# Optimization experiments

Measured on AMD Instinct MI355X. Metric: run time of the kernel, lower is better.

The kernel has to match this reference:

```python
import jax, jax.numpy as jnp
import numpy as np

N, I, H = 16, 128, 128
B, T = 16, 512


def setup_inputs() -> dict:
    key = jax.random.key(0)
    ks = jax.random.split(key, 6)
    stdv = 1.0 / np.sqrt(H)
    return {
        "x": jax.random.normal(ks[0], (B, T, N * I), dtype=jnp.float32),
        "h_0": jax.random.normal(ks[1], (1, B, N * H), dtype=jnp.float32),
        "weight_ih": jax.random.uniform(ks[2], (N, 3 * H, I), jnp.float32, -stdv, stdv),
        "weight_hh": jax.random.uniform(ks[3], (N, 3 * H, H), jnp.float32, -stdv, stdv),
        "bias_ih": jax.random.uniform(ks[4], (N, 3 * H), jnp.float32, -stdv, stdv),
        "bias_hh": jax.random.uniform(ks[5], (N, 3 * H), jnp.float32, -stdv, stdv),
    }


def reference(x, h_0, weight_ih, weight_hh, bias_ih, bias_hh):
    # x: [B, T, N*I] (batch_first)
    b, t, _ = x.shape
    xr = x.reshape(b, t, N, I)
    # Pre-compute all input projections: [B, T, N, 3H]
    gates_x = jnp.einsum('btni,ngi->btng', xr, weight_ih) + bias_ih[None, None]
    h0 = h_0[0].reshape(b, N, H)  # [B, N, H]

    def step(h, gx):
        # h: [B, N, H]; gx: [B, N, 3H]
        gates_h = jnp.einsum('bnh,ngh->bng', h, weight_hh) + bias_hh[None]
        gx_r, gx_z, gx_n = jnp.split(gx, 3, axis=-1)
        gh_r, gh_z, gh_n = jnp.split(gates_h, 3, axis=-1)
        r = jax.nn.sigmoid(gx_r + gh_r)
        z = jax.nn.sigmoid(gx_z + gh_z)
        n = jnp.tanh(gx_n + r * gh_n)
        h_new = (1 - z) * n + z * h
        return h_new, h_new

    # scan over time: gates_x -> [T, B, N, 3H]
    h_last, hs = jax.lax.scan(step, h0, jnp.swapaxes(gates_x, 0, 1))
    output = jnp.swapaxes(hs, 0, 1).reshape(b, t, N * H)  # [B, T, N*H]
    h_n = h_last.reshape(1, b, N * H)
    return output, h_n
```

## Files before the change

### kernel.cpp

```cpp
#include <hip/hip_runtime.h>
#include <cstdint>
#include <cmath>

#define N_HEADS 16
#define I_DIM 128
#define H_DIM 128
#define B_SZ 16
#define T_SZ 512
#define G3 384
#define BT (B_SZ * T_SZ)
#define LDW 136
#define OUT_HN_OFFSET ((size_t)B_SZ * T_SZ * (N_HEADS * H_DIM))
#define CHUNK 8
#define NCHUNK (T_SZ / CHUNK)

typedef __attribute__((ext_vector_type(8))) short bf16x8;
typedef __attribute__((ext_vector_type(4))) float f32x4;

static __device__ __forceinline__ unsigned short f2bf(float f) {
  unsigned int u = __float_as_uint(f);
  unsigned int r = (u + 0x7FFFu + ((u >> 16) & 1u)) >> 16;
  return (unsigned short)r;
}
static __device__ __forceinline__ float bf2f(unsigned short s) {
  return __uint_as_float((unsigned int)s << 16);
}
static __device__ __forceinline__ uint2 pack4(float4 v) {
  uint2 p;
  p.x = (unsigned int)f2bf(v.x) | ((unsigned int)f2bf(v.y) << 16);
  p.y = (unsigned int)f2bf(v.z) | ((unsigned int)f2bf(v.w) << 16);
  return p;
}
static __device__ __forceinline__ bf16x8 pack8(float4 a, float4 b) {
  union { uint2 u[2]; bf16x8 v; } r;
  r.u[0] = pack4(a);
  r.u[1] = pack4(b);
  return r.v;
}

__global__ __launch_bounds__(256) void gates_x_mfma(
    const float* __restrict__ x, const float* __restrict__ w_ih,
    const float* __restrict__ b_ih, unsigned short* __restrict__ gates) {
  const int n = blockIdx.z;
  const int grp = blockIdx.x;
  const int tid = threadIdx.x;
  const int wave = tid >> 6;
  const int lane = tid & 63;
  const int m16 = lane & 15;
  const int quad = lane >> 4;

  extern __shared__ __align__(16) unsigned short lds_pool[];
  unsigned short* Ws = lds_pool;
  unsigned short* Xs = lds_pool + G3 * LDW;

  const int xrow = tid >> 2;
  const int xq = tid & 3;

  float4 xf[8];
  {
    const float4* xg =
        (const float4*)(x + (size_t)(grp * 512 + xrow) * 2048 + n * I_DIM) +
        xq * 8;
#pragma unroll
    for (int i = 0; i < 8; ++i) xf[i] = xg[i];
  }

  {
    const float4* wsrc = (const float4*)(w_ih + (size_t)n * G3 * I_DIM);
#pragma unroll
    for (int i = 0; i < 48; ++i) {
      const int idx = i * 256 + tid;
      *(uint2*)&Ws[(idx >> 5) * LDW + (idx & 31) * 4] = pack4(wsrc[idx]);
    }
  }

  float bias[3][8];
#pragma unroll
  for (int gb = 0; gb < 3; ++gb)
#pragma unroll
    for (int j = 0; j < 8; ++j)
      bias[gb][j] = b_ih[n * G3 + gb * 128 + j * 16 + m16];

  for (int tile = 0; tile < 8; ++tile) {
    const int bt0 = grp * 512 + tile * 64;

    __syncthreads();
#pragma unroll
    for (int i = 0; i < 8; ++i)
      *(uint2*)&Xs[xrow * LDW + xq * 32 + i * 4] = pack4(xf[i]);
    __syncthreads();

    if (tile < 7) {
      const float4* xg =
          (const float4*)(x + (size_t)(bt0 + 64 + xrow) * 2048 + n * I_DIM) +
          xq * 8;
#pragma unroll
      for (int i = 0; i < 8; ++i) xf[i] = xg[i];
    }

#pragma unroll
    for (int gb = 0; gb < 3; ++gb) {
      f32x4 acc[8];
#pragma unroll
      for (int j = 0; j < 8; ++j) acc[j] = (f32x4){0.f, 0.f, 0.f, 0.f};

#pragma unroll
      for (int kt = 0; kt < 4; ++kt) {
        const bf16x8 afrag =
            *(const bf16x8*)&Xs[(wave * 16 + m16) * LDW + kt * 32 + quad * 8];
#pragma unroll
        for (int j = 0; j < 8; ++j) {
          const bf16x8 bfrag =
              *(const bf16x8*)&Ws[(gb * 128 + j * 16 + m16) * LDW + kt * 32 +
                                  quad * 8];
          acc[j] = __builtin_amdgcn_mfma_f32_16x16x32_bf16(afrag, bfrag,
                                                           acc[j], 0, 0, 0);
        }
      }

#pragma unroll
      for (int j = 0; j < 8; ++j) {
        const int g = gb * 128 + j * 16 + m16;
        float4 v;
        v.x = acc[j][0] + bias[gb][j];
        v.y = acc[j][1] + bias[gb][j];
        v.z = acc[j][2] + bias[gb][j];
        v.w = acc[j][3] + bias[gb][j];
        const int bt = bt0 + wave * 16 + quad * 4;
        *(uint2*)&gates[((size_t)n * G3 + g) * BT + bt] = pack4(v);
      }
    }
  }
}

__global__ __launch_bounds__(256, 1) void gru_scan_kernel(
    const float* __restrict__ h0, const float* __restrict__ w_hh,
    const float* __restrict__ b_hh, const unsigned short* __restrict__ gates,
    float* __restrict__ out) {
  const int b = blockIdx.x >> 4;
  const int n = blockIdx.x & 15;
  const int tid = threadIdx.x;
  const int wave = tid >> 6;
  const int lane = tid & 63;
  const int m16 = lane & 15;
  const int quad = lane >> 4;

  __shared__ __align__(16) unsigned short h2[2][2][H_DIM];
  __shared__ __align__(16) unsigned short gbuf[2][CHUNK * 512];

  bf16x8 wf[6][4];
  {
    const int cb0 = 2 * wave;
    const int cbs[6] = {cb0, 8 + cb0, 16 + cb0, cb0 + 1, 9 + cb0, 17 + cb0};
#pragma unroll
    for (int j = 0; j < 6; ++j) {
      const int g = cbs[j] * 16 + m16;
      const float4* wr = (const float4*)(w_hh + ((size_t)n * G3 + g) * H_DIM);
#pragma unroll
      for (int kt = 0; kt < 4; ++kt)
        wf[j][kt] = pack8(wr[kt * 8 + quad * 2], wr[kt * 8 + quad * 2 + 1]);
    }
  }

  const bool upd = quad < 2;
  const int elem = wave * 32 + quad * 16 + m16;

  float bh_r = 0.f, bh_z = 0.f, bh_n = 0.f, h_old = 0.f;
  if (upd) {
    bh_r = b_hh[n * G3 + elem];
    bh_z = b_hh[n * G3 + elem + 128];
    bh_n = b_hh[n * G3 + elem + 256];
    h_old = h0[(size_t)b * 2048 + n * H_DIM + elem];
    const unsigned short hh = f2bf(h_old);
    h2[0][0][elem] = hh;
    h2[0][1][elem] = f2bf(h_old - bf2f(hh));
  }

  const size_t grow0 = ((size_t)n * G3 + tid) * BT + (size_t)b * T_SZ;
  const size_t grow1 = ((size_t)n * G3 + 256 + tid) * BT + (size_t)b * T_SZ;

  auto scatter = [&](unsigned short* buf, int g, uint4 v) {
    unsigned short* d = buf + (g & 127) * 4 + (g >> 7);
    d[0]    = (unsigned short)v.x;
    d[512]  = (unsigned short)(v.x >> 16);
    d[1024] = (unsigned short)v.y;
    d[1536] = (unsigned short)(v.y >> 16);
    d[2048] = (unsigned short)v.z;
    d[2560] = (unsigned short)(v.z >> 16);
    d[3072] = (unsigned short)v.w;
    d[3584] = (unsigned short)(v.w >> 16);
  };

  uint4 pfA, pfB;
  pfA = *(const uint4*)(gates + grow0);
  if (tid < 128) pfB = *(const uint4*)(gates + grow1);
  scatter(gbuf[0], tid, pfA);
  if (tid < 128) scatter(gbuf[0], 256 + tid, pfB);
  __syncthreads();

  float* out_base = out + (size_t)b * T_SZ * 2048 + n * H_DIM;
  float oreg[CHUNK];

  for (int c = 0; c < NCHUNK; ++c) {
    const int gb = c & 1;

    if (c + 1 < NCHUNK) {
      pfA = *(const uint4*)(gates + grow0 + (size_t)(c + 1) * CHUNK);
      if (tid < 128)
        pfB = *(const uint4*)(gates + grow1 + (size_t)(c + 1) * CHUNK);
    }

#pragma unroll
    for (int s = 0; s < CHUNK; ++s) {
      const int rb = s & 1;
      const int wb = rb ^ 1;

      uint2 gxu = {0u, 0u};
      if (upd) gxu = *(const uint2*)&gbuf[gb][s * 512 + elem * 4];
      const float gxr = __uint_as_float(gxu.x << 16);
      const float gxz = __uint_as_float(gxu.x & 0xffff0000u);
      const float gxn = __uint_as_float(gxu.y << 16);

      const unsigned short* hsrc = &h2[rb][m16 & 1][0];
      const bf16x8 av0 = *(const bf16x8*)&hsrc[0 * 32 + quad * 8];
      const bf16x8 av1 = *(const bf16x8*)&hsrc[1 * 32 + quad * 8];
      const bf16x8 av2 = *(const bf16x8*)&hsrc[2 * 32 + quad * 8];
      const bf16x8 av3 = *(const bf16x8*)&hsrc[3 * 32 + quad * 8];

      f32x4 acc[6];
#pragma unroll
      for (int j = 0; j < 6; ++j) acc[j] = (f32x4){0.f, 0.f, 0.f, 0.f};
#pragma unroll
      for (int j = 0; j < 6; ++j)
        acc[j] = __builtin_amdgcn_mfma_f32_16x16x32_bf16(av0, wf[j][0],
                                                         acc[j], 0, 0, 0);
#pragma unroll
      for (int j = 0; j < 6; ++j)
        acc[j] = __builtin_amdgcn_mfma_f32_16x16x32_bf16(av1, wf[j][1],
                                                         acc[j], 0, 0, 0);
#pragma unroll
      for (int j = 0; j < 6; ++j)
        acc[j] = __builtin_amdgcn_mfma_f32_16x16x32_bf16(av2, wf[j][2],
                                                         acc[j], 0, 0, 0);
#pragma unroll
      for (int j = 0; j < 6; ++j)
        acc[j] = __builtin_amdgcn_mfma_f32_16x16x32_bf16(av3, wf[j][3],
                                                         acc[j], 0, 0, 0);

      if (upd) {
        const float ghr =
            (quad ? acc[3][0] + acc[3][1] : acc[0][0] + acc[0][1]) + bh_r;
        const float ghz =
            (quad ? acc[4][0] + acc[4][1] : acc[1][0] + acc[1][1]) + bh_z;
        const float ghn =
            (quad ? acc[5][0] + acc[5][1] : acc[2][0] + acc[2][1]) + bh_n;
        const float r = 1.f / (1.f + __expf(-(gxr + ghr)));
        const float z = 1.f / (1.f + __expf(-(gxz + ghz)));
        const float targ = gxn + r * ghn;
        const float rt = 1.f / (1.f + __expf(-2.f * targ));
        const float nn = 2.f * rt - 1.f;
        const float hn = (1.f - z) * nn + z * h_old;
        const unsigned short hh = f2bf(hn);
        h2[wb][0][elem] = hh;
        h2[wb][1][elem] = f2bf(hn - bf2f(hh));
        h_old = hn;
        oreg[s] = hn;
      }

      if (s == CHUNK - 1 && c + 1 < NCHUNK) {
        scatter(gbuf[gb ^ 1], tid, pfA);
        if (tid < 128) scatter(gbuf[gb ^ 1], 256 + tid, pfB);
      }
      __syncthreads();
    }

    if (upd) {
#pragma unroll
      for (int s = 0; s < CHUNK; ++s)
        out_base[(size_t)(c * CHUNK + s) * 2048 + elem] = oreg[s];
    }
  }

  if (upd) {
    out[OUT_HN_OFFSET + (size_t)b * 2048 + n * H_DIM + elem] = h_old;
  }
}

extern "C" void kernel_launch(void* const* d_in, const int* in_sizes, int n_in,
                              void* d_out, int out_size, void* d_ws,
                              size_t ws_size, hipStream_t stream) {
  const float* x    = (const float*)d_in[0];
  const float* h0   = (const float*)d_in[1];
  const float* w_ih = (const float*)d_in[2];
  const float* w_hh = (const float*)d_in[3];
  const float* b_ih = (const float*)d_in[4];
  const float* b_hh = (const float*)d_in[5];
  float* out = (float*)d_out;
  unsigned short* gates = (unsigned short*)d_ws;

  static bool lds_opt_in = false;
  if (!lds_opt_in) {
    (void)hipFuncSetAttribute(reinterpret_cast<const void*>(&gates_x_mfma),
                              hipFuncAttributeMaxDynamicSharedMemorySize,
                              (G3 + 64) * LDW * (int)sizeof(unsigned short));
    lds_opt_in = true;
  }

  dim3 gridA(16, 1, N_HEADS);
  gates_x_mfma<<<gridA, 256, (G3 + 64) * LDW * sizeof(unsigned short),
                 stream>>>(x, w_ih, b_ih, gates);
  gru_scan_kernel<<<256, 256, 0, stream>>>(h0, w_hh, b_hh, gates, out);
}
```

Before: 422.7 us.

## Keep input weights in registers and double waves in the scan kernel

```diff
diff --git a/kernel.cpp b/kernel.cpp
--- a/kernel.cpp
+++ b/kernel.cpp
@@ -38,7 +38,7 @@
   return r.v;
 }
 
-__global__ __launch_bounds__(256) void gates_x_mfma(
+__global__ __launch_bounds__(256, 2) void gates_x_mfma(
     const float* __restrict__ x, const float* __restrict__ w_ih,
     const float* __restrict__ b_ih, unsigned short* __restrict__ gates) {
   const int n = blockIdx.z;
@@ -49,9 +49,7 @@
   const int m16 = lane & 15;
   const int quad = lane >> 4;
 
-  extern __shared__ __align__(16) unsigned short lds_pool[];
-  unsigned short* Ws = lds_pool;
-  unsigned short* Xs = lds_pool + G3 * LDW;
+  __shared__ __align__(16) unsigned short Xs[64 * LDW];
 
   const int xrow = tid >> 2;
   const int xq = tid & 3;
@@ -59,30 +57,29 @@
   float4 xf[8];
   {
     const float4* xg =
-        (const float4*)(x + (size_t)(grp * 512 + xrow) * 2048 + n * I_DIM) +
+        (const float4*)(x + (size_t)(grp * 256 + xrow) * 2048 + n * I_DIM) +
         xq * 8;
 #pragma unroll
     for (int i = 0; i < 8; ++i) xf[i] = xg[i];
   }
 
-  {
-    const float4* wsrc = (const float4*)(w_ih + (size_t)n * G3 * I_DIM);
-#pragma unroll
-    for (int i = 0; i < 48; ++i) {
-      const int idx = i * 256 + tid;
-      *(uint2*)&Ws[(idx >> 5) * LDW + (idx & 31) * 4] = pack4(wsrc[idx]);
-    }
-  }
-
-  float bias[3][8];
-#pragma unroll
-  for (int gb = 0; gb < 3; ++gb)
-#pragma unroll
-    for (int j = 0; j < 8; ++j)
-      bias[gb][j] = b_ih[n * G3 + gb * 128 + j * 16 + m16];
-
-  for (int tile = 0; tile < 8; ++tile) {
-    const int bt0 = grp * 512 + tile * 64;
+  bf16x8 wfr[3][2][4];
+  float bias[3][2];
+#pragma unroll
+  for (int gb = 0; gb < 3; ++gb) {
+#pragma unroll
+    for (int jj = 0; jj < 2; ++jj) {
+      const int g = gb * 128 + (2 * wave + jj) * 16 + m16;
+      const float4* wr = (const float4*)(w_ih + ((size_t)n * G3 + g) * I_DIM);
+#pragma unroll
+      for (int kt = 0; kt < 4; ++kt)
+        wfr[gb][jj][kt] = pack8(wr[kt * 8 + quad * 2], wr[kt * 8 + quad * 2 + 1]);
+      bias[gb][jj] = b_ih[n * G3 + g];
+    }
+  }
+
+  for (int tile = 0; tile < 4; ++tile) {
+    const int bt0 = grp * 256 + tile * 64;
 
     __syncthreads();
 #pragma unroll
@@ -90,7 +87,7 @@
       *(uint2*)&Xs[xrow * LDW + xq * 32 + i * 4] = pack4(xf[i]);
     __syncthreads();
 
-    if (tile < 7) {
+    if (tile < 3) {
       const float4* xg =
           (const float4*)(x + (size_t)(bt0 + 64 + xrow) * 2048 + n * I_DIM) +
           xq * 8;
@@ -100,40 +97,45 @@
 
 #pragma unroll
     for (int gb = 0; gb < 3; ++gb) {
-      f32x4 acc[8];
-#pragma unroll
-      for (int j = 0; j < 8; ++j) acc[j] = (f32x4){0.f, 0.f, 0.f, 0.f};
+      f32x4 acc[4][2];
+#pragma unroll
+      for (int m = 0; m < 4; ++m)
+#pragma unroll
+        for (int jj = 0; jj < 2; ++jj) acc[m][jj] = (f32x4){0.f, 0.f, 0.f, 0.f};
 
 #pragma unroll
       for (int kt = 0; kt < 4; ++kt) {
-        const bf16x8 afrag =
-            *(const bf16x8*)&Xs[(wave * 16 + m16) * LDW + kt * 32 + quad * 8];
-#pragma unroll
-        for (int j = 0; j < 8; ++j) {
-          const bf16x8 bfrag =
-              *(const bf16x8*)&Ws[(gb * 128 + j * 16 + m16) * LDW + kt * 32 +
-                                  quad * 8];
-          acc[j] = __builtin_amdgcn_mfma_f32_16x16x32_bf16(afrag, bfrag,
-                                                           acc[j], 0, 0, 0);
+        bf16x8 af[4];
+#pragma unroll
+        for (int m = 0; m < 4; ++m)
+          af[m] = *(const bf16x8*)&Xs[(m * 16 + m16) * LDW + kt * 32 + quad * 8];
+#pragma unroll
+        for (int m = 0; m < 4; ++m)
+#pragma unroll
+          for (int jj = 0; jj < 2; ++jj)
+            acc[m][jj] = __builtin_amdgcn_mfma_f32_16x16x32_bf16(
+                af[m], wfr[gb][jj][kt], acc[m][jj], 0, 0, 0);
+      }
+
+#pragma unroll
+      for (int m = 0; m < 4; ++m) {
+#pragma unroll
+        for (int jj = 0; jj < 2; ++jj) {
+          const int g = gb * 128 + (2 * wave + jj) * 16 + m16;
+          float4 v;
+          v.x = acc[m][jj][0] + bias[gb][jj];
+          v.y = acc[m][jj][1] + bias[gb][jj];
+          v.z = acc[m][jj][2] + bias[gb][jj];
+          v.w = acc[m][jj][3] + bias[gb][jj];
+          const int bt = bt0 + m * 16 + quad * 4;
+          *(uint2*)&gates[((size_t)n * G3 + g) * BT + bt] = pack4(v);
         }
       }
-
-#pragma unroll
-      for (int j = 0; j < 8; ++j) {
-        const int g = gb * 128 + j * 16 + m16;
-        float4 v;
-        v.x = acc[j][0] + bias[gb][j];
-        v.y = acc[j][1] + bias[gb][j];
-        v.z = acc[j][2] + bias[gb][j];
-        v.w = acc[j][3] + bias[gb][j];
-        const int bt = bt0 + wave * 16 + quad * 4;
-        *(uint2*)&gates[((size_t)n * G3 + g) * BT + bt] = pack4(v);
-      }
-    }
-  }
-}
-
-__global__ __launch_bounds__(256, 1) void gru_scan_kernel(
+    }
+  }
+}
+
+__global__ __launch_bounds__(512, 1) void gru_scan_kernel(
     const float* __restrict__ h0, const float* __restrict__ w_hh,
     const float* __restrict__ b_hh, const unsigned short* __restrict__ gates,
     float* __restrict__ out) {
@@ -148,12 +150,11 @@
   __shared__ __align__(16) unsigned short h2[2][2][H_DIM];
   __shared__ __align__(16) unsigned short gbuf[2][CHUNK * 512];
 
-  bf16x8 wf[6][4];
+  bf16x8 wf[3][4];
   {
-    const int cb0 = 2 * wave;
-    const int cbs[6] = {cb0, 8 + cb0, 16 + cb0, cb0 + 1, 9 + cb0, 17 + cb0};
-#pragma unroll
-    for (int j = 0; j < 6; ++j) {
+    const int cbs[3] = {wave, 8 + wave, 16 + wave};
+#pragma unroll
+    for (int j = 0; j < 3; ++j) {
       const int g = cbs[j] * 16 + m16;
       const float4* wr = (const float4*)(w_hh + ((size_t)n * G3 + g) * H_DIM);
 #pragma unroll
@@ -162,8 +163,8 @@
     }
   }
 
-  const bool upd = quad < 2;
-  const int elem = wave * 32 + quad * 16 + m16;
+  const bool upd = (quad == 0);
+  const int elem = wave * 16 + m16;
 
   float bh_r = 0.f, bh_z = 0.f, bh_n = 0.f, h_old = 0.f;
   if (upd) {
@@ -176,8 +177,7 @@
     h2[0][1][elem] = f2bf(h_old - bf2f(hh));
   }
 
-  const size_t grow0 = ((size_t)n * G3 + tid) * BT + (size_t)b * T_SZ;
-  const size_t grow1 = ((size_t)n * G3 + 256 + tid) * BT + (size_t)b * T_SZ;
+  const size_t grow = ((size_t)n * G3 + tid) * BT + (size_t)b * T_SZ;
 
   auto scatter = [&](unsigned short* buf, int g, uint4 v) {
     unsigned short* d = buf + (g & 127) * 4 + (g >> 7);
@@ -191,11 +191,11 @@
     d[3584] = (unsigned short)(v.w >> 16);
   };
 
-  uint4 pfA, pfB;
-  pfA = *(const uint4*)(gates + grow0);
-  if (tid < 128) pfB = *(const uint4*)(gates + grow1);
-  scatter(gbuf[0], tid, pfA);
-  if (tid < 128) scatter(gbuf[0], 256 + tid, pfB);
+  uint4 pfA = {0, 0, 0, 0};
+  if (tid < G3) {
+    pfA = *(const uint4*)(gates + grow);
+    scatter(gbuf[0], tid, pfA);
+  }
   __syncthreads();
 
   float* out_base = out + (size_t)b * T_SZ * 2048 + n * H_DIM;
@@ -204,11 +204,8 @@
   for (int c = 0; c < NCHUNK; ++c) {
     const int gb = c & 1;
 
-    if (c + 1 < NCHUNK) {
-      pfA = *(const uint4*)(gates + grow0 + (size_t)(c + 1) * CHUNK);
-      if (tid < 128)
-        pfB = *(const uint4*)(gates + grow1 + (size_t)(c + 1) * CHUNK);
-    }
+    if (c + 1 < NCHUNK && tid < G3)
+      pfA = *(const uint4*)(gates + grow + (size_t)(c + 1) * CHUNK);
 
 #pragma unroll
     for (int s = 0; s < CHUNK; ++s) {
@@ -227,33 +224,26 @@
       const bf16x8 av2 = *(const bf16x8*)&hsrc[2 * 32 + quad * 8];
       const bf16x8 av3 = *(const bf16x8*)&hsrc[3 * 32 + quad * 8];
 
-      f32x4 acc[6];
-#pragma unroll
-      for (int j = 0; j < 6; ++j) acc[j] = (f32x4){0.f, 0.f, 0.f, 0.f};
-#pragma unroll
-      for (int j = 0; j < 6; ++j)
-        acc[j] = __builtin_amdgcn_mfma_f32_16x16x32_bf16(av0, wf[j][0],
-                                                         acc[j], 0, 0, 0);
-#pragma unroll
-      for (int j = 0; j < 6; ++j)
-        acc[j] = __builtin_amdgcn_mfma_f32_16x16x32_bf16(av1, wf[j][1],
-                                                         acc[j], 0, 0, 0);
-#pragma unroll
-      for (int j = 0; j < 6; ++j)
-        acc[j] = __builtin_amdgcn_mfma_f32_16x16x32_bf16(av2, wf[j][2],
-                                                         acc[j], 0, 0, 0);
-#pragma unroll
-      for (int j = 0; j < 6; ++j)
-        acc[j] = __builtin_amdgcn_mfma_f32_16x16x32_bf16(av3, wf[j][3],
-                                                         acc[j], 0, 0, 0);
+      f32x4 a0 = {0.f, 0.f, 0.f, 0.f};
+      f32x4 a1 = {0.f, 0.f, 0.f, 0.f};
+      f32x4 a2 = {0.f, 0.f, 0.f, 0.f};
+      a0 = __builtin_amdgcn_mfma_f32_16x16x32_bf16(av0, wf[0][0], a0, 0, 0, 0);
+      a1 = __builtin_amdgcn_mfma_f32_16x16x32_bf16(av0, wf[1][0], a1, 0, 0, 0);
+      a2 = __builtin_amdgcn_mfma_f32_16x16x32_bf16(av0, wf[2][0], a2, 0, 0, 0);
+      a0 = __builtin_amdgcn_mfma_f32_16x16x32_bf16(av1, wf[0][1], a0, 0, 0, 0);
+      a1 = __builtin_amdgcn_mfma_f32_16x16x32_bf16(av1, wf[1][1], a1, 0, 0, 0);
+      a2 = __builtin_amdgcn_mfma_f32_16x16x32_bf16(av1, wf[2][1], a2, 0, 0, 0);
+      a0 = __builtin_amdgcn_mfma_f32_16x16x32_bf16(av2, wf[0][2], a0, 0, 0, 0);
+      a1 = __builtin_amdgcn_mfma_f32_16x16x32_bf16(av2, wf[1][2], a1, 0, 0, 0);
+      a2 = __builtin_amdgcn_mfma_f32_16x16x32_bf16(av2, wf[2][2], a2, 0, 0, 0);
+      a0 = __builtin_amdgcn_mfma_f32_16x16x32_bf16(av3, wf[0][3], a0, 0, 0, 0);
+      a1 = __builtin_amdgcn_mfma_f32_16x16x32_bf16(av3, wf[1][3], a1, 0, 0, 0);
+      a2 = __builtin_amdgcn_mfma_f32_16x16x32_bf16(av3, wf[2][3], a2, 0, 0, 0);
 
       if (upd) {
-        const float ghr =
-            (quad ? acc[3][0] + acc[3][1] : acc[0][0] + acc[0][1]) + bh_r;
-        const float ghz =
-            (quad ? acc[4][0] + acc[4][1] : acc[1][0] + acc[1][1]) + bh_z;
-        const float ghn =
-            (quad ? acc[5][0] + acc[5][1] : acc[2][0] + acc[2][1]) + bh_n;
+        const float ghr = a0[0] + a0[1] + bh_r;
+        const float ghz = a1[0] + a1[1] + bh_z;
+        const float ghn = a2[0] + a2[1] + bh_n;
         const float r = 1.f / (1.f + __expf(-(gxr + ghr)));
         const float z = 1.f / (1.f + __expf(-(gxz + ghz)));
         const float targ = gxn + r * ghn;
@@ -267,10 +257,8 @@
         oreg[s] = hn;
       }
 
-      if (s == CHUNK - 1 && c + 1 < NCHUNK) {
+      if (s == CHUNK - 1 && c + 1 < NCHUNK && tid < G3)
         scatter(gbuf[gb ^ 1], tid, pfA);
-        if (tid < 128) scatter(gbuf[gb ^ 1], 256 + tid, pfB);
-      }
       __syncthreads();
     }
 
@@ -298,16 +286,7 @@
   float* out = (float*)d_out;
   unsigned short* gates = (unsigned short*)d_ws;
 
-  static bool lds_opt_in = false;
-  if (!lds_opt_in) {
-    (void)hipFuncSetAttribute(reinterpret_cast<const void*>(&gates_x_mfma),
-                              hipFuncAttributeMaxDynamicSharedMemorySize,
-                              (G3 + 64) * LDW * (int)sizeof(unsigned short));
-    lds_opt_in = true;
-  }
-
-  dim3 gridA(16, 1, N_HEADS);
-  gates_x_mfma<<<gridA, 256, (G3 + 64) * LDW * sizeof(unsigned short),
-                 stream>>>(x, w_ih, b_ih, gates);
-  gru_scan_kernel<<<256, 256, 0, stream>>>(h0, w_hh, b_hh, gates, out);
-}
+  dim3 gridA(32, 1, N_HEADS);
+  gates_x_mfma<<<gridA, 256, 0, stream>>>(x, w_ih, b_ih, gates);
+  gru_scan_kernel<<<256, 512, 0, stream>>>(h0, w_hh, b_hh, gates, out);
+}
```

Result: slower. 433.0 us (+2.4%).

## Fuse input-gate projection into the GRU scan kernel per chunk

Applied to the files above, without the earlier changes.

```diff
diff --git a/kernel.cpp b/kernel.cpp
--- a/kernel.cpp
+++ b/kernel.cpp
@@ -8,11 +8,10 @@
 #define B_SZ 16
 #define T_SZ 512
 #define G3 384
-#define BT (B_SZ * T_SZ)
-#define LDW 136
 #define OUT_HN_OFFSET ((size_t)B_SZ * T_SZ * (N_HEADS * H_DIM))
 #define CHUNK 8
 #define NCHUNK (T_SZ / CHUNK)
+#define HPAD 160
 
 typedef __attribute__((ext_vector_type(8))) short bf16x8;
 typedef __attribute__((ext_vector_type(4))) float f32x4;
@@ -38,104 +37,10 @@
   return r.v;
 }
 
-__global__ __launch_bounds__(256) void gates_x_mfma(
-    const float* __restrict__ x, const float* __restrict__ w_ih,
-    const float* __restrict__ b_ih, unsigned short* __restrict__ gates) {
-  const int n = blockIdx.z;
-  const int grp = blockIdx.x;
-  const int tid = threadIdx.x;
-  const int wave = tid >> 6;
-  const int lane = tid & 63;
-  const int m16 = lane & 15;
-  const int quad = lane >> 4;
-
-  extern __shared__ __align__(16) unsigned short lds_pool[];
-  unsigned short* Ws = lds_pool;
-  unsigned short* Xs = lds_pool + G3 * LDW;
-
-  const int xrow = tid >> 2;
-  const int xq = tid & 3;
-
-  float4 xf[8];
-  {
-    const float4* xg =
-        (const float4*)(x + (size_t)(grp * 512 + xrow) * 2048 + n * I_DIM) +
-        xq * 8;
-#pragma unroll
-    for (int i = 0; i < 8; ++i) xf[i] = xg[i];
-  }
-
-  {
-    const float4* wsrc = (const float4*)(w_ih + (size_t)n * G3 * I_DIM);
-#pragma unroll
-    for (int i = 0; i < 48; ++i) {
-      const int idx = i * 256 + tid;
-      *(uint2*)&Ws[(idx >> 5) * LDW + (idx & 31) * 4] = pack4(wsrc[idx]);
-    }
-  }
-
-  float bias[3][8];
-#pragma unroll
-  for (int gb = 0; gb < 3; ++gb)
-#pragma unroll
-    for (int j = 0; j < 8; ++j)
-      bias[gb][j] = b_ih[n * G3 + gb * 128 + j * 16 + m16];
-
-  for (int tile = 0; tile < 8; ++tile) {
-    const int bt0 = grp * 512 + tile * 64;
-
-    __syncthreads();
-#pragma unroll
-    for (int i = 0; i < 8; ++i)
-      *(uint2*)&Xs[xrow * LDW + xq * 32 + i * 4] = pack4(xf[i]);
-    __syncthreads();
-
-    if (tile < 7) {
-      const float4* xg =
-          (const float4*)(x + (size_t)(bt0 + 64 + xrow) * 2048 + n * I_DIM) +
-          xq * 8;
-#pragma unroll
-      for (int i = 0; i < 8; ++i) xf[i] = xg[i];
-    }
-
-#pragma unroll
-    for (int gb = 0; gb < 3; ++gb) {
-      f32x4 acc[8];
-#pragma unroll
-      for (int j = 0; j < 8; ++j) acc[j] = (f32x4){0.f, 0.f, 0.f, 0.f};
-
-#pragma unroll
-      for (int kt = 0; kt < 4; ++kt) {
-        const bf16x8 afrag =
-            *(const bf16x8*)&Xs[(wave * 16 + m16) * LDW + kt * 32 + quad * 8];
-#pragma unroll
-        for (int j = 0; j < 8; ++j) {
-          const bf16x8 bfrag =
-              *(const bf16x8*)&Ws[(gb * 128 + j * 16 + m16) * LDW + kt * 32 +
-                                  quad * 8];
-          acc[j] = __builtin_amdgcn_mfma_f32_16x16x32_bf16(afrag, bfrag,
-                                                           acc[j], 0, 0, 0);
-        }
-      }
-
-#pragma unroll
-      for (int j = 0; j < 8; ++j) {
-        const int g = gb * 128 + j * 16 + m16;
-        float4 v;
-        v.x = acc[j][0] + bias[gb][j];
-        v.y = acc[j][1] + bias[gb][j];
-        v.z = acc[j][2] + bias[gb][j];
-        v.w = acc[j][3] + bias[gb][j];
-        const int bt = bt0 + wave * 16 + quad * 4;
-        *(uint2*)&gates[((size_t)n * G3 + g) * BT + bt] = pack4(v);
-      }
-    }
-  }
-}
-
-__global__ __launch_bounds__(256, 1) void gru_scan_kernel(
-    const float* __restrict__ h0, const float* __restrict__ w_hh,
-    const float* __restrict__ b_hh, const unsigned short* __restrict__ gates,
+__global__ __launch_bounds__(256, 1) void gru_fused_kernel(
+    const float* __restrict__ x, const float* __restrict__ h0,
+    const float* __restrict__ w_ih, const float* __restrict__ w_hh,
+    const float* __restrict__ b_ih, const float* __restrict__ b_hh,
     float* __restrict__ out) {
   const int b = blockIdx.x >> 4;
   const int n = blockIdx.x & 15;
@@ -145,8 +50,8 @@
   const int m16 = lane & 15;
   const int quad = lane >> 4;
 
-  __shared__ __align__(16) unsigned short h2[2][2][H_DIM];
-  __shared__ __align__(16) unsigned short gbuf[2][CHUNK * 512];
+  __shared__ __align__(16) unsigned short h2[2][2][HPAD];
+  __shared__ __align__(16) float gbuf[2][CHUNK][512];
 
   bf16x8 wf[6][4];
   {
@@ -162,13 +67,24 @@
     }
   }
 
+  bf16x8 wxf[6][4];
+#pragma unroll
+  for (int jj = 0; jj < 6; ++jj) {
+    const int g = (wave * 6 + jj) * 16 + m16;
+    const float4* wr = (const float4*)(w_ih + ((size_t)n * G3 + g) * I_DIM);
+#pragma unroll
+    for (int kt = 0; kt < 4; ++kt)
+      wxf[jj][kt] = pack8(wr[kt * 8 + quad * 2], wr[kt * 8 + quad * 2 + 1]);
+  }
+
   const bool upd = quad < 2;
   const int elem = wave * 32 + quad * 16 + m16;
 
-  float bh_r = 0.f, bh_z = 0.f, bh_n = 0.f, h_old = 0.f;
+  float bs_r = 0.f, bs_z = 0.f, bs_n = 0.f, bh_n = 0.f, h_old = 0.f;
   if (upd) {
-    bh_r = b_hh[n * G3 + elem];
-    bh_z = b_hh[n * G3 + elem + 128];
+    bs_r = b_ih[n * G3 + elem] + b_hh[n * G3 + elem];
+    bs_z = b_ih[n * G3 + elem + 128] + b_hh[n * G3 + elem + 128];
+    bs_n = b_ih[n * G3 + elem + 256];
     bh_n = b_hh[n * G3 + elem + 256];
     h_old = h0[(size_t)b * 2048 + n * H_DIM + elem];
     const unsigned short hh = f2bf(h_old);
@@ -176,26 +92,42 @@
     h2[0][1][elem] = f2bf(h_old - bf2f(hh));
   }
 
-  const size_t grow0 = ((size_t)n * G3 + tid) * BT + (size_t)b * T_SZ;
-  const size_t grow1 = ((size_t)n * G3 + 256 + tid) * BT + (size_t)b * T_SZ;
-
-  auto scatter = [&](unsigned short* buf, int g, uint4 v) {
-    unsigned short* d = buf + (g & 127) * 4 + (g >> 7);
-    d[0]    = (unsigned short)v.x;
-    d[512]  = (unsigned short)(v.x >> 16);
-    d[1024] = (unsigned short)v.y;
-    d[1536] = (unsigned short)(v.y >> 16);
-    d[2048] = (unsigned short)v.z;
-    d[2560] = (unsigned short)(v.z >> 16);
-    d[3072] = (unsigned short)v.w;
-    d[3584] = (unsigned short)(v.w >> 16);
-  };
-
-  uint4 pfA, pfB;
-  pfA = *(const uint4*)(gates + grow0);
-  if (tid < 128) pfB = *(const uint4*)(gates + grow1);
-  scatter(gbuf[0], tid, pfA);
-  if (tid < 128) scatter(gbuf[0], 256 + tid, pfB);
+  const float* xrow_base = x + (size_t)b * T_SZ * 2048 + n * I_DIM +
+                           (size_t)(m16 & 7) * 2048 + quad * 8;
+
+  float4 pf[8];
+
+#define LOAD_X_CHUNK(c)                                                       \
+  {                                                                           \
+    const float* xr = xrow_base + (size_t)(c) * CHUNK * 2048;                 \
+    _Pragma("unroll") for (int kt = 0; kt < 4; ++kt) {                        \
+      pf[kt * 2] = *(const float4*)(xr + kt * 32);                            \
+      pf[kt * 2 + 1] = *(const float4*)(xr + kt * 32 + 4);                    \
+    }                                                                         \
+  }
+
+#define GATES_X_CHUNK(gdst)                                                   \
+  {                                                                           \
+    bf16x8 af[4];                                                             \
+    _Pragma("unroll") for (int kt = 0; kt < 4; ++kt)                          \
+        af[kt] = pack8(pf[kt * 2], pf[kt * 2 + 1]);                           \
+    _Pragma("unroll") for (int jj = 0; jj < 6; ++jj) {                        \
+      f32x4 a = {0.f, 0.f, 0.f, 0.f};                                         \
+      _Pragma("unroll") for (int kt = 0; kt < 4; ++kt)                        \
+          a = __builtin_amdgcn_mfma_f32_16x16x32_bf16(af[kt], wxf[jj][kt], a, \
+                                                      0, 0, 0);               \
+      if (quad < 2) {                                                         \
+        const int g = (wave * 6 + jj) * 16 + m16;                             \
+        const int e4 = (g & 127) * 4 + (g >> 7);                              \
+        _Pragma("unroll") for (int r = 0; r < 4; ++r)                         \
+            (gdst)[(quad * 4 + r) * 512 + e4] = a[r];                         \
+      }                                                                       \
+    }                                                                         \
+  }
+
+  LOAD_X_CHUNK(0);
+  GATES_X_CHUNK(&gbuf[0][0][0]);
+  LOAD_X_CHUNK(1);
   __syncthreads();
 
   float* out_base = out + (size_t)b * T_SZ * 2048 + n * H_DIM;
@@ -205,9 +137,8 @@
     const int gb = c & 1;
 
     if (c + 1 < NCHUNK) {
-      pfA = *(const uint4*)(gates + grow0 + (size_t)(c + 1) * CHUNK);
-      if (tid < 128)
-        pfB = *(const uint4*)(gates + grow1 + (size_t)(c + 1) * CHUNK);
+      GATES_X_CHUNK(&gbuf[gb ^ 1][0][0]);
+      if (c + 2 < NCHUNK) LOAD_X_CHUNK(c + 2);
     }
 
 #pragma unroll
@@ -215,11 +146,13 @@
       const int rb = s & 1;
       const int wb = rb ^ 1;
 
-      uint2 gxu = {0u, 0u};
-      if (upd) gxu = *(const uint2*)&gbuf[gb][s * 512 + elem * 4];
-      const float gxr = __uint_as_float(gxu.x << 16);
-      const float gxz = __uint_as_float(gxu.x & 0xffff0000u);
-      const float gxn = __uint_as_float(gxu.y << 16);
+      float gxr = 0.f, gxz = 0.f, gxn = 0.f;
+      if (upd) {
+        const f32x4 g4 = *(const f32x4*)&gbuf[gb][s][elem * 4];
+        gxr = g4[0];
+        gxz = g4[1];
+        gxn = g4[2];
+      }
 
       const unsigned short* hsrc = &h2[rb][m16 & 1][0];
       const bf16x8 av0 = *(const bf16x8*)&hsrc[0 * 32 + quad * 8];
@@ -232,31 +165,31 @@
       for (int j = 0; j < 6; ++j) acc[j] = (f32x4){0.f, 0.f, 0.f, 0.f};
 #pragma unroll
       for (int j = 0; j < 6; ++j)
-        acc[j] = __builtin_amdgcn_mfma_f32_16x16x32_bf16(av0, wf[j][0],
-                                                         acc[j], 0, 0, 0);
-#pragma unroll
-      for (int j = 0; j < 6; ++j)
-        acc[j] = __builtin_amdgcn_mfma_f32_16x16x32_bf16(av1, wf[j][1],
-                                                         acc[j], 0, 0, 0);
-#pragma unroll
-      for (int j = 0; j < 6; ++j)
-        acc[j] = __builtin_amdgcn_mfma_f32_16x16x32_bf16(av2, wf[j][2],
-                                                         acc[j], 0, 0, 0);
-#pragma unroll
-      for (int j = 0; j < 6; ++j)
-        acc[j] = __builtin_amdgcn_mfma_f32_16x16x32_bf16(av3, wf[j][3],
-                                                         acc[j], 0, 0, 0);
+        acc[j] = __builtin_amdgcn_mfma_f32_16x16x32_bf16(av0, wf[j][0], acc[j],
+                                                         0, 0, 0);
+#pragma unroll
+      for (int j = 0; j < 6; ++j)
+        acc[j] = __builtin_amdgcn_mfma_f32_16x16x32_bf16(av1, wf[j][1], acc[j],
+                                                         0, 0, 0);
+#pragma unroll
+      for (int j = 0; j < 6; ++j)
+        acc[j] = __builtin_amdgcn_mfma_f32_16x16x32_bf16(av2, wf[j][2], acc[j],
+                                                         0, 0, 0);
+#pragma unroll
+      for (int j = 0; j < 6; ++j)
+        acc[j] = __builtin_amdgcn_mfma_f32_16x16x32_bf16(av3, wf[j][3], acc[j],
+                                                         0, 0, 0);
 
       if (upd) {
         const float ghr =
-            (quad ? acc[3][0] + acc[3][1] : acc[0][0] + acc[0][1]) + bh_r;
+            (quad ? acc[3][0] + acc[3][1] : acc[0][0] + acc[0][1]);
         const float ghz =
-            (quad ? acc[4][0] + acc[4][1] : acc[1][0] + acc[1][1]) + bh_z;
-        const float ghn =
-            (quad ? acc[5][0] + acc[5][1] : acc[2][0] + acc[2][1]) + bh_n;
-        const float r = 1.f / (1.f + __expf(-(gxr + ghr)));
-        const float z = 1.f / (1.f + __expf(-(gxz + ghz)));
-        const float targ = gxn + r * ghn;
+            (quad ? acc[4][0] + acc[4][1] : acc[1][0] + acc[1][1]);
+        const float ghn0 =
+            (quad ? acc[5][0] + acc[5][1] : acc[2][0] + acc[2][1]);
+        const float r = 1.f / (1.f + __expf(-(gxr + ghr + bs_r)));
+        const float z = 1.f / (1.f + __expf(-(gxz + ghz + bs_z)));
+        const float targ = gxn + bs_n + r * (ghn0 + bh_n);
         const float rt = 1.f / (1.f + __expf(-2.f * targ));
         const float nn = 2.f * rt - 1.f;
         const float hn = (1.f - z) * nn + z * h_old;
@@ -265,11 +198,6 @@
         h2[wb][1][elem] = f2bf(hn - bf2f(hh));
         h_old = hn;
         oreg[s] = hn;
-      }
-
-      if (s == CHUNK - 1 && c + 1 < NCHUNK) {
-        scatter(gbuf[gb ^ 1], tid, pfA);
-        if (tid < 128) scatter(gbuf[gb ^ 1], 256 + tid, pfB);
       }
       __syncthreads();
     }
@@ -296,18 +224,8 @@
   const float* b_ih = (const float*)d_in[4];
   const float* b_hh = (const float*)d_in[5];
   float* out = (float*)d_out;
-  unsigned short* gates = (unsigned short*)d_ws;
-
-  static bool lds_opt_in = false;
-  if (!lds_opt_in) {
-    (void)hipFuncSetAttribute(reinterpret_cast<const void*>(&gates_x_mfma),
-                              hipFuncAttributeMaxDynamicSharedMemorySize,
-                              (G3 + 64) * LDW * (int)sizeof(unsigned short));
-    lds_opt_in = true;
-  }
-
-  dim3 gridA(16, 1, N_HEADS);
-  gates_x_mfma<<<gridA, 256, (G3 + 64) * LDW * sizeof(unsigned short),
-                 stream>>>(x, w_ih, b_ih, gates);
-  gru_scan_kernel<<<256, 256, 0, stream>>>(h0, w_hh, b_hh, gates, out);
-}
+  (void)d_ws;
+
+  gru_fused_kernel<<<256, 256, 0, stream>>>(x, h0, w_ih, w_hh, b_ih, b_hh,
+                                            out);
+}
```

After: 431.6 us. 2.1% more time.
